# Kernel tuning notes

Hardware: AMD Instinct MI355X
Metric: run time of the kernel (lower is better)

## Reference

```python
import jax, jax.numpy as jnp
import numpy as np

D_MODEL = 512
NUM_HEADS = 8
D_K = D_MODEL // NUM_HEADS


def setup_inputs() -> dict:
    key = jax.random.key(0)
    ks = jax.random.split(key, 11)
    B, S = 2, 4096
    s = 1.0 / np.sqrt(D_MODEL)
    inp = {
        "q": jax.random.normal(ks[0], (B, S, D_MODEL), jnp.float32),
        "k": jax.random.normal(ks[1], (B, S, D_MODEL), jnp.float32),
        "v": jax.random.normal(ks[2], (B, S, D_MODEL), jnp.float32),
        "Wq": jax.random.normal(ks[3], (D_MODEL, D_MODEL), jnp.float32) * s,
        "bq": jnp.zeros((D_MODEL,), jnp.float32),
        "Wk": jax.random.normal(ks[4], (D_MODEL, D_MODEL), jnp.float32) * s,
        "bk": jnp.zeros((D_MODEL,), jnp.float32),
        "Wv": jax.random.normal(ks[5], (D_MODEL, D_MODEL), jnp.float32) * s,
        "bv": jnp.zeros((D_MODEL,), jnp.float32),
        "Wo": jax.random.normal(ks[6], (D_MODEL, D_MODEL), jnp.float32) * s,
        "bo": jnp.zeros((D_MODEL,), jnp.float32),
    }
    return inp


def reference(q, k, v, Wq, bq, Wk, bk, Wv, bv, Wo, bo):
    B, S, _ = q.shape
    # Linear projections (torch Linear: x @ W.T + b)
    def proj(x, W, b):
        y = jnp.einsum("bsd,ed->bse", x, W) + b
        return y.reshape(B, -1, NUM_HEADS, D_K).transpose(0, 2, 1, 3)  # [B,H,S,d_k]

    qh = proj(q, Wq, bq)
    kh = proj(k, Wk, bk)
    vh = proj(v, Wv, bv)

    scale = 1.0 / np.sqrt(D_K).astype(np.float32)
    scores = jnp.einsum("bhqd,bhkd->bhqk", qh, kh) * scale  # [B,H,S,S]
    attn = jax.nn.softmax(scores, axis=-1)
    ctx = jnp.einsum("bhqk,bhkd->bhqd", attn, vh)  # [B,H,S,d_k]
    ctx = ctx.transpose(0, 2, 1, 3).reshape(B, -1, D_MODEL)
    out = jnp.einsum("bsd,ed->bse", ctx, Wo) + bo
    return out
```

## Files before the change

### kernel.cpp

```cpp
#include <hip/hip_runtime.h>
#include <hip/hip_bf16.h>
#include <stdint.h>


typedef float  floatx4 __attribute__((ext_vector_type(4)));
typedef __bf16 bf16x8  __attribute__((ext_vector_type(8)));
typedef short  shortx4 __attribute__((ext_vector_type(4)));

#define MFMA16(a, b, c) __builtin_amdgcn_mfma_f32_16x16x32_bf16((a), (b), (c), 0, 0, 0)

#define QSCALE 0.1803368801111244f

__device__ __forceinline__ short f2bf(float f) {
  union { float f; uint32_t u; } a; a.f = f;
  uint32_t u = a.u;
  u += 0x7fffu + ((u >> 16) & 1u);
  return (short)(u >> 16);
}

__device__ __forceinline__ void stage16(const short* g, short* l) {
  __builtin_amdgcn_global_load_lds(
      (const __attribute__((address_space(1))) void*)g,
      (__attribute__((address_space(3))) void*)l, 16, 0, 0);
}

__global__ __launch_bounds__(256) void cvt3_kernel(const float* __restrict__ q,
                                                   const float* __restrict__ k,
                                                   const float* __restrict__ v,
                                                   short* __restrict__ out, int n4) {
  const int which = blockIdx.y;
  const float* in = which == 0 ? q : which == 1 ? k : v;
  short* o = out + (size_t)which * (size_t)n4 * 4;
  int i = blockIdx.x * 256 + threadIdx.x;
  if (i < n4) {
    float4 f = reinterpret_cast<const float4*>(in)[i];
    shortx4 s;
    s.x = f2bf(f.x); s.y = f2bf(f.y); s.z = f2bf(f.z); s.w = f2bf(f.w);
    reinterpret_cast<shortx4*>(o)[i] = s;
  }
}

__global__ __launch_bounds__(256) void cvtw_kernel(const float* __restrict__ w0,
                                                   const float* __restrict__ w1,
                                                   const float* __restrict__ w2,
                                                   const float* __restrict__ w3,
                                                   short* __restrict__ out, int n4) {
  const int which = blockIdx.y;
  const float* in = which == 0 ? w0 : which == 1 ? w1 : which == 2 ? w2 : w3;
  short* o = out + (size_t)which * (size_t)n4 * 4;
  int i = blockIdx.x * 256 + threadIdx.x;
  if (i < n4) {
    float4 f = reinterpret_cast<const float4*>(in)[i];
    shortx4 s;
    s.x = f2bf(f.x); s.y = f2bf(f.y); s.z = f2bf(f.z); s.w = f2bf(f.w);
    reinterpret_cast<shortx4*>(o)[i] = s;
  }
}

__global__ __launch_bounds__(256) void proj3_kernel(
    const short* __restrict__ xq, const short* __restrict__ xk, const short* __restrict__ xv,
    const short* __restrict__ wq, const short* __restrict__ wk, const short* __restrict__ wv,
    const float* __restrict__ bq, const float* __restrict__ bk, const float* __restrict__ bv,
    short* __restrict__ Qh, short* __restrict__ KV) {
  const int which = blockIdx.z;
  const short* A = which == 0 ? xq : which == 1 ? xk : xv;
  const short* W = which == 0 ? wq : which == 1 ? wk : wv;
  const float* bias = which == 0 ? bq : which == 1 ? bk : bv;

  __shared__ __align__(16) short sA[2][4096];
  __shared__ __align__(16) short sB[2][2048];

  const int K = 512;
  const int tid = threadIdx.x;
  const int lane = tid & 63;
  const int wave = tid >> 6;
  const int l15 = lane & 15;
  const int quad = lane >> 4;
  const int tileM = blockIdx.x * 128;
  const int tileN = blockIdx.y * 64;

  const int srow = tid >> 2;
  const int fr = (srow ^ (srow >> 2)) & 3;
  const int sq = ((tid & 3) ^ fr) * 8;
  const short* As0 = A + (size_t)(tileM + srow) * K + sq;
  const short* As1 = As0 + (size_t)64 * K;
  const short* Bs  = W + (size_t)(tileN + srow) * K + sq;
  const int ldw = wave * 512;

  const int fl = (l15 ^ (l15 >> 2)) & 3;
  const int qsw = (quad ^ fl) * 8;
  const int ra0 = (wave * 32 + l15) * 32 + qsw;
  const int ra1 = ra0 + 512;
  const int rb0 = l15 * 32 + qsw;

  floatx4 acc[2][4];
#pragma unroll
  for (int mt = 0; mt < 2; ++mt)
#pragma unroll
    for (int nt = 0; nt < 4; ++nt) acc[mt][nt] = (floatx4){0.f, 0.f, 0.f, 0.f};

  stage16(As0, &sA[0][ldw]);
  stage16(As1, &sA[0][2048 + ldw]);
  stage16(Bs,  &sB[0][ldw]);

#pragma unroll 2
  for (int t = 0; t < 16; ++t) {
    __syncthreads();
    if (t != 15) {
      const int kk = (t + 1) * 32;
      short* a_ld = &sA[(t + 1) & 1][ldw];
      stage16(As0 + kk, a_ld);
      stage16(As1 + kk, a_ld + 2048);
      stage16(Bs + kk, &sB[(t + 1) & 1][ldw]);
    }
    const short* sa = sA[t & 1];
    const short* sb = sB[t & 1];
    bf16x8 a0 = *(const bf16x8*)&sa[ra0];
    bf16x8 a1 = *(const bf16x8*)&sa[ra1];
#pragma unroll
    for (int nt = 0; nt < 4; ++nt) {
      bf16x8 wf = *(const bf16x8*)&sb[rb0 + nt * 512];
      acc[0][nt] = MFMA16(a0, wf, acc[0][nt]);
      acc[1][nt] = MFMA16(a1, wf, acc[1][nt]);
    }
  }

#pragma unroll
  for (int mt = 0; mt < 2; ++mt) {
    const int rowbase = tileM + wave * 32 + mt * 16 + quad * 4;
    const int b = rowbase >> 12, s = rowbase & 4095;
    const int g = s >> 5;
    if (which == 0) {
#pragma unroll
      for (int nt = 0; nt < 4; ++nt) {
        const int col = tileN + nt * 16 + l15;
        const int h = col >> 6, d = col & 63;
        const float bc = bias[col];
#pragma unroll
        for (int r = 0; r < 4; ++r) {
          const int row = rowbase + r;
          const int ss = row & 4095;
          Qh[(size_t)((b * 8 + h) * 4096 + ss) * 64 + d] = f2bf((acc[mt][nt][r] + bc) * QSCALE);
        }
      }
    } else if (which == 1) {
      const int key = s & 31;
      const int t = key >> 4;
      const int l15b = key & 15;
#pragma unroll
      for (int nt = 0; nt < 4; ++nt) {
        const int col = tileN + nt * 16 + l15;
        const int h = col >> 6, dd = col & 63;
        const int ks = dd >> 5, quadk = (dd >> 3) & 3, jj = dd & 7;
        const float bc = bias[col];
        const size_t base = ((size_t)(b * 8 + h) * 128 + g) * 4096 +
                            (size_t)(t * 2 + ks) * 512 + (size_t)quadk * 128 + jj;
#pragma unroll
        for (int r = 0; r < 4; ++r)
          KV[base + (size_t)(l15b + r) * 8] = f2bf(acc[mt][nt][r] + bc);
      }
    } else {
      const int p32 = s & 31;
      const int l0 = ((p32 & 15) >> 2) * 8 + (p32 >> 4) * 4;
      const int quadv = l0 >> 3, jv = l0 & 7;
#pragma unroll
      for (int nt = 0; nt < 4; ++nt) {
        const int col = tileN + nt * 16 + l15;
        const int h = col >> 6, dd = col & 63;
        const int dt = dd >> 4, l15v = dd & 15;
        const float bc = bias[col];
        shortx4 p;
        p.x = f2bf(acc[mt][nt][0] + bc);
        p.y = f2bf(acc[mt][nt][1] + bc);
        p.z = f2bf(acc[mt][nt][2] + bc);
        p.w = f2bf(acc[mt][nt][3] + bc);
        *(shortx4*)(KV + ((size_t)(b * 8 + h) * 128 + g) * 4096 + 2048 +
                    (size_t)dt * 512 + (size_t)quadv * 128 + (size_t)l15v * 8 + jv) = p;
      }
    }
  }
}

__global__ __launch_bounds__(256) void proj_o_kernel(
    const short* __restrict__ A, const short* __restrict__ W,
    const float* __restrict__ bias, float* __restrict__ out) {
  __shared__ __align__(16) short sA[2][4096];
  __shared__ __align__(16) short sB[2][2048];

  const int K = 512;
  const int tid = threadIdx.x;
  const int lane = tid & 63;
  const int wave = tid >> 6;
  const int l15 = lane & 15;
  const int quad = lane >> 4;
  const int tileM = blockIdx.x * 128;
  const int tileN = blockIdx.y * 64;

  const int srow = tid >> 2;
  const int fr = (srow ^ (srow >> 2)) & 3;
  const int sq = ((tid & 3) ^ fr) * 8;
  const short* As0 = A + (size_t)(tileM + srow) * K + sq;
  const short* As1 = As0 + (size_t)64 * K;
  const short* Bs  = W + (size_t)(tileN + srow) * K + sq;
  const int ldw = wave * 512;

  const int fl = (l15 ^ (l15 >> 2)) & 3;
  const int qsw = (quad ^ fl) * 8;
  const int ra0 = (wave * 32 + l15) * 32 + qsw;
  const int ra1 = ra0 + 512;
  const int rb0 = l15 * 32 + qsw;

  floatx4 acc[2][4];
#pragma unroll
  for (int mt = 0; mt < 2; ++mt)
#pragma unroll
    for (int nt = 0; nt < 4; ++nt) acc[mt][nt] = (floatx4){0.f, 0.f, 0.f, 0.f};

  stage16(As0, &sA[0][ldw]);
  stage16(As1, &sA[0][2048 + ldw]);
  stage16(Bs,  &sB[0][ldw]);

#pragma unroll 2
  for (int t = 0; t < 16; ++t) {
    __syncthreads();
    if (t != 15) {
      const int kk = (t + 1) * 32;
      short* a_ld = &sA[(t + 1) & 1][ldw];
      stage16(As0 + kk, a_ld);
      stage16(As1 + kk, a_ld + 2048);
      stage16(Bs + kk, &sB[(t + 1) & 1][ldw]);
    }
    const short* sa = sA[t & 1];
    const short* sb = sB[t & 1];
    bf16x8 a0 = *(const bf16x8*)&sa[ra0];
    bf16x8 a1 = *(const bf16x8*)&sa[ra1];
#pragma unroll
    for (int nt = 0; nt < 4; ++nt) {
      bf16x8 wf = *(const bf16x8*)&sb[rb0 + nt * 512];
      acc[0][nt] = MFMA16(a0, wf, acc[0][nt]);
      acc[1][nt] = MFMA16(a1, wf, acc[1][nt]);
    }
  }

#pragma unroll
  for (int mt = 0; mt < 2; ++mt) {
    const int rowbase = tileM + wave * 32 + mt * 16 + quad * 4;
#pragma unroll
    for (int nt = 0; nt < 4; ++nt) {
      const int col = tileN + nt * 16 + l15;
      const float bc = bias[col];
#pragma unroll
      for (int r = 0; r < 4; ++r) out[(size_t)(rowbase + r) * 512 + col] = acc[mt][nt][r] + bc;
    }
  }
}

__global__ __launch_bounds__(512) void flash_kernel(
    const short* __restrict__ Qh, const short* __restrict__ KV,
    short* __restrict__ ctx) {
  __shared__ __align__(16) short sKV[2][8192];
  __shared__ float comb[4][64][34];

  const int id = blockIdx.x;
  const int xcd = id & 7;
  const int j = id >> 3;
  const int bh = xcd + ((j >> 5) << 3);
  const int qtile = j & 31;

  const int tid = threadIdx.x;
  const int wave = tid >> 6;
  const int lane = tid & 63;
  const int l15 = lane & 15;
  const int quad = lane >> 4;
  const int wq = wave & 3;
  const int half = wave >> 2;
  const int qrow0 = qtile * 128 + wq * 32;

  bf16x8 qf[2][2];
#pragma unroll
  for (int nt = 0; nt < 2; ++nt) {
    const short* Qb = Qh + (size_t)(bh * 4096 + qrow0 + nt * 16 + l15) * 64 + quad * 8;
    qf[nt][0] = *(const bf16x8*)(Qb);
    qf[nt][1] = *(const bf16x8*)(Qb + 32);
  }

  bf16x8 ones;
  {
    union { short s[8]; bf16x8 v; } u;
#pragma unroll
    for (int i = 0; i < 8; ++i) u.s[i] = (short)0x3F80;
    ones = u.v;
  }

  const short* KVb = KV + (size_t)bh * (128 * 4096);
  const short* sg = KVb + wave * 512 + lane * 8;
  const int ldw = wave * 512;

  const floatx4 FZ = (floatx4){0.f, 0.f, 0.f, 0.f};
  floatx4 o[2][4];
  floatx4 lacc[2];
#pragma unroll
  for (int nt = 0; nt < 2; ++nt) {
    lacc[nt] = FZ;
#pragma unroll
    for (int dt = 0; dt < 4; ++dt) o[nt][dt] = FZ;
  }

  stage16(sg, &sKV[0][ldw]);
  stage16(sg + 4096, &sKV[0][ldw + 4096]);

#define COMPUTE(S) do {                                                         \
    bf16x8 ka[2][2], vf[4];                                                     \
    ka[0][0] = *(const bf16x8*)&(S)[av];                                        \
    ka[0][1] = *(const bf16x8*)&(S)[av + 512];                                  \
    ka[1][0] = *(const bf16x8*)&(S)[av + 1024];                                 \
    ka[1][1] = *(const bf16x8*)&(S)[av + 1536];                                 \
    vf[0] = *(const bf16x8*)&(S)[av + 2048];                                    \
    vf[1] = *(const bf16x8*)&(S)[av + 2560];                                    \
    vf[2] = *(const bf16x8*)&(S)[av + 3072];                                    \
    vf[3] = *(const bf16x8*)&(S)[av + 3584];                                    \
    floatx4 st[2][2];                                                           \
    _Pragma("unroll")                                                           \
    for (int nt = 0; nt < 2; ++nt)                                              \
      _Pragma("unroll")                                                         \
      for (int t = 0; t < 2; ++t)                                               \
        st[nt][t] = MFMA16(ka[t][1], qf[nt][1], MFMA16(ka[t][0], qf[nt][0], FZ)); \
    bf16x8 pb[2];                                                               \
    _Pragma("unroll")                                                           \
    for (int nt = 0; nt < 2; ++nt) {                                            \
      float p[8];                                                               \
      _Pragma("unroll")                                                         \
      for (int t = 0; t < 2; ++t)                                               \
        _Pragma("unroll")                                                       \
        for (int r = 0; r < 4; ++r) p[t * 4 + r] = __builtin_amdgcn_exp2f(st[nt][t][r]); \
      union { __hip_bfloat162 h2[4]; bf16x8 v8; } u;                            \
      u.h2[0] = __float22bfloat162_rn(float2{p[0], p[1]});                      \
      u.h2[1] = __float22bfloat162_rn(float2{p[2], p[3]});                      \
      u.h2[2] = __float22bfloat162_rn(float2{p[4], p[5]});                      \
      u.h2[3] = __float22bfloat162_rn(float2{p[6], p[7]});                      \
      pb[nt] = u.v8;                                                            \
    }                                                                           \
    _Pragma("unroll")                                                           \
    for (int nt = 0; nt < 2; ++nt) {                                            \
      lacc[nt] = MFMA16(ones, pb[nt], lacc[nt]);                                \
      _Pragma("unroll")                                                         \
      for (int dt = 0; dt < 4; ++dt)                                            \
        o[nt][dt] = MFMA16(vf[dt], pb[nt], o[nt][dt]);                          \
    }                                                                           \
  } while (0)

  const int av = lane * 8;

  for (int it = 0; it < 64; ++it) {
    __syncthreads();

    if (it != 63) {
      const short* gs = sg + (size_t)(2 * it + 2) * 4096;
      short* ld = &sKV[(it + 1) & 1][ldw];
      stage16(gs, ld);
      stage16(gs + 4096, ld + 4096);
    }

    const short* S = sKV[it & 1] + (half << 12);
    COMPUTE(S);
  }
#undef COMPUTE

  __syncthreads();
  if (half) {
    float* cb = comb[wq][lane];
#pragma unroll
    for (int nt = 0; nt < 2; ++nt) {
#pragma unroll
      for (int dt = 0; dt < 4; ++dt)
#pragma unroll
        for (int r = 0; r < 4; ++r) cb[nt * 16 + dt * 4 + r] = o[nt][dt][r];
      cb[32 + nt] = lacc[nt][0];
    }
  }
  __syncthreads();
  if (!half) {
    const float* cb = comb[wq][lane];
    const int b = bh >> 3, h = bh & 7;
#pragma unroll
    for (int nt = 0; nt < 2; ++nt) {
      const float inv = 1.0f / (lacc[nt][0] + cb[32 + nt]);
      const int row = qrow0 + nt * 16 + l15;
      short* cp = ctx + (size_t)(b * 4096 + row) * 512 + h * 64 + quad * 4;
#pragma unroll
      for (int dt = 0; dt < 4; ++dt) {
        union { __hip_bfloat162 h2[2]; shortx4 s4; } u;
        u.h2[0] = __float22bfloat162_rn(
            float2{(o[nt][dt][0] + cb[nt * 16 + dt * 4 + 0]) * inv,
                   (o[nt][dt][1] + cb[nt * 16 + dt * 4 + 1]) * inv});
        u.h2[1] = __float22bfloat162_rn(
            float2{(o[nt][dt][2] + cb[nt * 16 + dt * 4 + 2]) * inv,
                   (o[nt][dt][3] + cb[nt * 16 + dt * 4 + 3]) * inv});
        *(shortx4*)(cp + dt * 16) = u.s4;
      }
    }
  }
}

extern "C" void kernel_launch(void* const* d_in, const int* in_sizes, int n_in,
                              void* d_out, int out_size, void* d_ws, size_t ws_size,
                              hipStream_t stream) {
  const float* q  = (const float*)d_in[0];
  const float* k  = (const float*)d_in[1];
  const float* v  = (const float*)d_in[2];
  const float* Wq = (const float*)d_in[3];
  const float* bq = (const float*)d_in[4];
  const float* Wk = (const float*)d_in[5];
  const float* bk = (const float*)d_in[6];
  const float* Wv = (const float*)d_in[7];
  const float* bv = (const float*)d_in[8];
  const float* Wo = (const float*)d_in[9];
  const float* bo = (const float*)d_in[10];

  const int XN = 2 * 4096 * 512;
  const int WN = 512 * 512;

  short* ws  = (short*)d_ws;
  short* xqb = ws;
  short* xkb = ws + (size_t)XN;
  short* xvb = ws + (size_t)2 * XN;
  short* wqb = ws + (size_t)3 * XN;
  short* wkb = wqb + WN;
  short* wvb = wkb + WN;
  short* wob = wvb + WN;
  short* Qh  = wob + WN;
  short* KVf = Qh + (size_t)XN;
  short* ctx = xqb;

  dim3 cg(XN / 4 / 256, 3);
  cvt3_kernel<<<cg, 256, 0, stream>>>(q, k, v, xqb, XN / 4);
  dim3 wg(WN / 4 / 256, 4);
  cvtw_kernel<<<wg, 256, 0, stream>>>(Wq, Wk, Wv, Wo, wqb, WN / 4);

  dim3 pg(64, 8, 3);
  proj3_kernel<<<pg, 256, 0, stream>>>(xqb, xkb, xvb, wqb, wkb, wvb,
                                       bq, bk, bv, Qh, KVf);

  flash_kernel<<<512, 512, 0, stream>>>(Qh, KVf, ctx);

  dim3 og(64, 8);
  proj_o_kernel<<<og, 256, 0, stream>>>(ctx, wob, bo, (float*)d_out);
}
```

Before: 212.7 us.

## Merge conversion kernels, widen GEMM N tiles, split flash KV four ways

Merges the activation and weight bf16 conversion kernels into one launch. Doubles the N tile of the projection GEMMs to 128 columns, which halves the grid and reuses each A fragment across more MFMAs at the cost of more accumulator registers. Moves the flash kernel to 1024 threads with a four-way split of each KV block across wave groups, and combines the partial outputs through a tree reduction in LDS that reuses the KV buffer. This raises in-flight work per block but adds reduction syncs and register pressure under the launch_bounds(1024, 8) hint.

```diff
diff --git a/kernel.cpp b/kernel.cpp
--- a/kernel.cpp
+++ b/kernel.cpp
@@ -24,37 +24,33 @@
       (__attribute__((address_space(3))) void*)l, 16, 0, 0);
 }
 
-__global__ __launch_bounds__(256) void cvt3_kernel(const float* __restrict__ q,
-                                                   const float* __restrict__ k,
-                                                   const float* __restrict__ v,
-                                                   short* __restrict__ out, int n4) {
-  const int which = blockIdx.y;
-  const float* in = which == 0 ? q : which == 1 ? k : v;
-  short* o = out + (size_t)which * (size_t)n4 * 4;
-  int i = blockIdx.x * 256 + threadIdx.x;
-  if (i < n4) {
-    float4 f = reinterpret_cast<const float4*>(in)[i];
-    shortx4 s;
-    s.x = f2bf(f.x); s.y = f2bf(f.y); s.z = f2bf(f.z); s.w = f2bf(f.w);
-    reinterpret_cast<shortx4*>(o)[i] = s;
-  }
-}
-
-__global__ __launch_bounds__(256) void cvtw_kernel(const float* __restrict__ w0,
-                                                   const float* __restrict__ w1,
-                                                   const float* __restrict__ w2,
-                                                   const float* __restrict__ w3,
-                                                   short* __restrict__ out, int n4) {
-  const int which = blockIdx.y;
-  const float* in = which == 0 ? w0 : which == 1 ? w1 : which == 2 ? w2 : w3;
-  short* o = out + (size_t)which * (size_t)n4 * 4;
-  int i = blockIdx.x * 256 + threadIdx.x;
-  if (i < n4) {
-    float4 f = reinterpret_cast<const float4*>(in)[i];
-    shortx4 s;
-    s.x = f2bf(f.x); s.y = f2bf(f.y); s.z = f2bf(f.z); s.w = f2bf(f.w);
-    reinterpret_cast<shortx4*>(o)[i] = s;
-  }
+__global__ __launch_bounds__(256) void cvt_all_kernel(
+    const float* __restrict__ q, const float* __restrict__ k, const float* __restrict__ v,
+    const float* __restrict__ Wq, const float* __restrict__ Wk,
+    const float* __restrict__ Wv, const float* __restrict__ Wo,
+    short* __restrict__ act, short* __restrict__ wts) {
+  const int A4 = (2 * 4096 * 512) / 4;
+  const int W4 = (512 * 512) / 4;
+  const int i = blockIdx.x * 256 + threadIdx.x;
+  const float* in;
+  short* out;
+  int j;
+  if (i < 3 * A4) {
+    const int which = i >> 20;
+    j = i - which * A4;
+    in = which == 0 ? q : which == 1 ? k : v;
+    out = act + (size_t)which * (size_t)A4 * 4;
+  } else {
+    const int t = i - 3 * A4;
+    const int which = t >> 16;
+    j = t - which * W4;
+    in = which == 0 ? Wq : which == 1 ? Wk : which == 2 ? Wv : Wo;
+    out = wts + (size_t)which * (size_t)W4 * 4;
+  }
+  float4 f = reinterpret_cast<const float4*>(in)[j];
+  shortx4 s;
+  s.x = f2bf(f.x); s.y = f2bf(f.y); s.z = f2bf(f.z); s.w = f2bf(f.w);
+  reinterpret_cast<shortx4*>(out)[j] = s;
 }
 
 __global__ __launch_bounds__(256) void proj3_kernel(
@@ -68,7 +64,7 @@
   const float* bias = which == 0 ? bq : which == 1 ? bk : bv;
 
   __shared__ __align__(16) short sA[2][4096];
-  __shared__ __align__(16) short sB[2][2048];
+  __shared__ __align__(16) short sB[2][4096];
 
   const int K = 512;
   const int tid = threadIdx.x;
@@ -77,14 +73,15 @@
   const int l15 = lane & 15;
   const int quad = lane >> 4;
   const int tileM = blockIdx.x * 128;
-  const int tileN = blockIdx.y * 64;
+  const int tileN = blockIdx.y * 128;
 
   const int srow = tid >> 2;
   const int fr = (srow ^ (srow >> 2)) & 3;
   const int sq = ((tid & 3) ^ fr) * 8;
   const short* As0 = A + (size_t)(tileM + srow) * K + sq;
   const short* As1 = As0 + (size_t)64 * K;
-  const short* Bs  = W + (size_t)(tileN + srow) * K + sq;
+  const short* Bs0 = W + (size_t)(tileN + srow) * K + sq;
+  const short* Bs1 = Bs0 + (size_t)64 * K;
   const int ldw = wave * 512;
 
   const int fl = (l15 ^ (l15 >> 2)) & 3;
@@ -93,15 +90,16 @@
   const int ra1 = ra0 + 512;
   const int rb0 = l15 * 32 + qsw;
 
-  floatx4 acc[2][4];
+  floatx4 acc[2][8];
 #pragma unroll
   for (int mt = 0; mt < 2; ++mt)
 #pragma unroll
-    for (int nt = 0; nt < 4; ++nt) acc[mt][nt] = (floatx4){0.f, 0.f, 0.f, 0.f};
+    for (int nt = 0; nt < 8; ++nt) acc[mt][nt] = (floatx4){0.f, 0.f, 0.f, 0.f};
 
   stage16(As0, &sA[0][ldw]);
   stage16(As1, &sA[0][2048 + ldw]);
-  stage16(Bs,  &sB[0][ldw]);
+  stage16(Bs0, &sB[0][ldw]);
+  stage16(Bs1, &sB[0][2048 + ldw]);
 
 #pragma unroll 2
   for (int t = 0; t < 16; ++t) {
@@ -109,16 +107,18 @@
     if (t != 15) {
       const int kk = (t + 1) * 32;
       short* a_ld = &sA[(t + 1) & 1][ldw];
+      short* b_ld = &sB[(t + 1) & 1][ldw];
       stage16(As0 + kk, a_ld);
       stage16(As1 + kk, a_ld + 2048);
-      stage16(Bs + kk, &sB[(t + 1) & 1][ldw]);
+      stage16(Bs0 + kk, b_ld);
+      stage16(Bs1 + kk, b_ld + 2048);
     }
     const short* sa = sA[t & 1];
     const short* sb = sB[t & 1];
     bf16x8 a0 = *(const bf16x8*)&sa[ra0];
     bf16x8 a1 = *(const bf16x8*)&sa[ra1];
 #pragma unroll
-    for (int nt = 0; nt < 4; ++nt) {
+    for (int nt = 0; nt < 8; ++nt) {
       bf16x8 wf = *(const bf16x8*)&sb[rb0 + nt * 512];
       acc[0][nt] = MFMA16(a0, wf, acc[0][nt]);
       acc[1][nt] = MFMA16(a1, wf, acc[1][nt]);
@@ -132,7 +132,7 @@
     const int g = s >> 5;
     if (which == 0) {
 #pragma unroll
-      for (int nt = 0; nt < 4; ++nt) {
+      for (int nt = 0; nt < 8; ++nt) {
         const int col = tileN + nt * 16 + l15;
         const int h = col >> 6, d = col & 63;
         const float bc = bias[col];
@@ -145,16 +145,16 @@
       }
     } else if (which == 1) {
       const int key = s & 31;
-      const int t = key >> 4;
+      const int tt = key >> 4;
       const int l15b = key & 15;
 #pragma unroll
-      for (int nt = 0; nt < 4; ++nt) {
+      for (int nt = 0; nt < 8; ++nt) {
         const int col = tileN + nt * 16 + l15;
         const int h = col >> 6, dd = col & 63;
         const int ks = dd >> 5, quadk = (dd >> 3) & 3, jj = dd & 7;
         const float bc = bias[col];
         const size_t base = ((size_t)(b * 8 + h) * 128 + g) * 4096 +
-                            (size_t)(t * 2 + ks) * 512 + (size_t)quadk * 128 + jj;
+                            (size_t)(tt * 2 + ks) * 512 + (size_t)quadk * 128 + jj;
 #pragma unroll
         for (int r = 0; r < 4; ++r)
           KV[base + (size_t)(l15b + r) * 8] = f2bf(acc[mt][nt][r] + bc);
@@ -164,7 +164,7 @@
       const int l0 = ((p32 & 15) >> 2) * 8 + (p32 >> 4) * 4;
       const int quadv = l0 >> 3, jv = l0 & 7;
 #pragma unroll
-      for (int nt = 0; nt < 4; ++nt) {
+      for (int nt = 0; nt < 8; ++nt) {
         const int col = tileN + nt * 16 + l15;
         const int h = col >> 6, dd = col & 63;
         const int dt = dd >> 4, l15v = dd & 15;
@@ -185,7 +185,7 @@
     const short* __restrict__ A, const short* __restrict__ W,
     const float* __restrict__ bias, float* __restrict__ out) {
   __shared__ __align__(16) short sA[2][4096];
-  __shared__ __align__(16) short sB[2][2048];
+  __shared__ __align__(16) short sB[2][4096];
 
   const int K = 512;
   const int tid = threadIdx.x;
@@ -194,14 +194,15 @@
   const int l15 = lane & 15;
   const int quad = lane >> 4;
   const int tileM = blockIdx.x * 128;
-  const int tileN = blockIdx.y * 64;
+  const int tileN = blockIdx.y * 128;
 
   const int srow = tid >> 2;
   const int fr = (srow ^ (srow >> 2)) & 3;
   const int sq = ((tid & 3) ^ fr) * 8;
   const short* As0 = A + (size_t)(tileM + srow) * K + sq;
   const short* As1 = As0 + (size_t)64 * K;
-  const short* Bs  = W + (size_t)(tileN + srow) * K + sq;
+  const short* Bs0 = W + (size_t)(tileN + srow) * K + sq;
+  const short* Bs1 = Bs0 + (size_t)64 * K;
   const int ldw = wave * 512;
 
   const int fl = (l15 ^ (l15 >> 2)) & 3;
@@ -210,15 +211,16 @@
   const int ra1 = ra0 + 512;
   const int rb0 = l15 * 32 + qsw;
 
-  floatx4 acc[2][4];
+  floatx4 acc[2][8];
 #pragma unroll
   for (int mt = 0; mt < 2; ++mt)
 #pragma unroll
-    for (int nt = 0; nt < 4; ++nt) acc[mt][nt] = (floatx4){0.f, 0.f, 0.f, 0.f};
+    for (int nt = 0; nt < 8; ++nt) acc[mt][nt] = (floatx4){0.f, 0.f, 0.f, 0.f};
 
   stage16(As0, &sA[0][ldw]);
   stage16(As1, &sA[0][2048 + ldw]);
-  stage16(Bs,  &sB[0][ldw]);
+  stage16(Bs0, &sB[0][ldw]);
+  stage16(Bs1, &sB[0][2048 + ldw]);
 
 #pragma unroll 2
   for (int t = 0; t < 16; ++t) {
@@ -226,16 +228,18 @@
     if (t != 15) {
       const int kk = (t + 1) * 32;
       short* a_ld = &sA[(t + 1) & 1][ldw];
+      short* b_ld = &sB[(t + 1) & 1][ldw];
       stage16(As0 + kk, a_ld);
       stage16(As1 + kk, a_ld + 2048);
-      stage16(Bs + kk, &sB[(t + 1) & 1][ldw]);
+      stage16(Bs0 + kk, b_ld);
+      stage16(Bs1 + kk, b_ld + 2048);
     }
     const short* sa = sA[t & 1];
     const short* sb = sB[t & 1];
     bf16x8 a0 = *(const bf16x8*)&sa[ra0];
     bf16x8 a1 = *(const bf16x8*)&sa[ra1];
 #pragma unroll
-    for (int nt = 0; nt < 4; ++nt) {
+    for (int nt = 0; nt < 8; ++nt) {
       bf16x8 wf = *(const bf16x8*)&sb[rb0 + nt * 512];
       acc[0][nt] = MFMA16(a0, wf, acc[0][nt]);
       acc[1][nt] = MFMA16(a1, wf, acc[1][nt]);
@@ -246,7 +250,7 @@
   for (int mt = 0; mt < 2; ++mt) {
     const int rowbase = tileM + wave * 32 + mt * 16 + quad * 4;
 #pragma unroll
-    for (int nt = 0; nt < 4; ++nt) {
+    for (int nt = 0; nt < 8; ++nt) {
       const int col = tileN + nt * 16 + l15;
       const float bc = bias[col];
 #pragma unroll
@@ -255,11 +259,11 @@
   }
 }
 
-__global__ __launch_bounds__(512) void flash_kernel(
+__global__ __launch_bounds__(1024, 8) void flash_kernel(
     const short* __restrict__ Qh, const short* __restrict__ KV,
     short* __restrict__ ctx) {
-  __shared__ __align__(16) short sKV[2][8192];
-  __shared__ float comb[4][64][34];
+  __shared__ __align__(16) short sKV[2][16384];
+  __shared__ float comb_l[3][4][64][2];
 
   const int id = blockIdx.x;
   const int xcd = id & 7;
@@ -272,9 +276,9 @@
   const int lane = tid & 63;
   const int l15 = lane & 15;
   const int quad = lane >> 4;
-  const int wq = wave & 3;
-  const int half = wave >> 2;
-  const int qrow0 = qtile * 128 + wq * 32;
+  const int qg = wave & 3;
+  const int ks = wave >> 2;
+  const int qrow0 = qtile * 128 + qg * 32;
 
   bf16x8 qf[2][2];
 #pragma unroll
@@ -293,8 +297,8 @@
   }
 
   const short* KVb = KV + (size_t)bh * (128 * 4096);
-  const short* sg = KVb + wave * 512 + lane * 8;
-  const int ldw = wave * 512;
+  const short* sg = KVb + wave * 1024 + lane * 8;
+  const int ldw = wave * 1024;
 
   const floatx4 FZ = (floatx4){0.f, 0.f, 0.f, 0.f};
   floatx4 o[2][4];
@@ -307,7 +311,7 @@
   }
 
   stage16(sg, &sKV[0][ldw]);
-  stage16(sg + 4096, &sKV[0][ldw + 4096]);
+  stage16(sg + 512, &sKV[0][ldw + 512]);
 
 #define COMPUTE(S) do {                                                         \
     bf16x8 ka[2][2], vf[4];                                                     \
@@ -351,51 +355,85 @@
 
   const int av = lane * 8;
 
-  for (int it = 0; it < 64; ++it) {
+  for (int it = 0; it < 32; ++it) {
     __syncthreads();
 
-    if (it != 63) {
-      const short* gs = sg + (size_t)(2 * it + 2) * 4096;
+    if (it != 31) {
+      const short* gs = sg + (size_t)(it + 1) * 16384;
       short* ld = &sKV[(it + 1) & 1][ldw];
       stage16(gs, ld);
-      stage16(gs + 4096, ld + 4096);
-    }
-
-    const short* S = sKV[it & 1] + (half << 12);
+      stage16(gs + 512, ld + 512);
+    }
+
+    const short* S = &sKV[it & 1][ks << 12];
     COMPUTE(S);
   }
 #undef COMPUTE
 
   __syncthreads();
-  if (half) {
-    float* cb = comb[wq][lane];
+  float* cb = (float*)sKV;
+  const int slot = (qg * 64 + lane) * 32;
+  const int rot = lane & 7;
+
+  if (ks == 1 || ks == 3) {
+    float* dst = cb + (ks == 3 ? 8192 : 0) + slot;
+#pragma unroll
+    for (int nt = 0; nt < 2; ++nt)
+#pragma unroll
+      for (int dt = 0; dt < 4; ++dt) {
+        const int c = nt * 4 + dt;
+        *(floatx4*)(dst + ((c ^ rot) & 7) * 4) = o[nt][dt];
+      }
+  }
+  if (ks) {
+    comb_l[ks - 1][qg][lane][0] = lacc[0][0];
+    comb_l[ks - 1][qg][lane][1] = lacc[1][0];
+  }
+  __syncthreads();
+  if (ks == 0 || ks == 2) {
+    const float* src = cb + (ks == 2 ? 8192 : 0) + slot;
+#pragma unroll
+    for (int nt = 0; nt < 2; ++nt)
+#pragma unroll
+      for (int dt = 0; dt < 4; ++dt) {
+        const int c = nt * 4 + dt;
+        o[nt][dt] += *(const floatx4*)(src + ((c ^ rot) & 7) * 4);
+      }
+  }
+  __syncthreads();
+  if (ks == 2) {
+    float* dst = cb + slot;
+#pragma unroll
+    for (int nt = 0; nt < 2; ++nt)
+#pragma unroll
+      for (int dt = 0; dt < 4; ++dt) {
+        const int c = nt * 4 + dt;
+        *(floatx4*)(dst + ((c ^ rot) & 7) * 4) = o[nt][dt];
+      }
+  }
+  __syncthreads();
+  if (ks == 0) {
+    const float* src = cb + slot;
+#pragma unroll
+    for (int nt = 0; nt < 2; ++nt)
+#pragma unroll
+      for (int dt = 0; dt < 4; ++dt) {
+        const int c = nt * 4 + dt;
+        o[nt][dt] += *(const floatx4*)(src + ((c ^ rot) & 7) * 4);
+      }
+    const int b = bh >> 3, h = bh & 7;
 #pragma unroll
     for (int nt = 0; nt < 2; ++nt) {
-#pragma unroll
-      for (int dt = 0; dt < 4; ++dt)
-#pragma unroll
-        for (int r = 0; r < 4; ++r) cb[nt * 16 + dt * 4 + r] = o[nt][dt][r];
-      cb[32 + nt] = lacc[nt][0];
-    }
-  }
-  __syncthreads();
-  if (!half) {
-    const float* cb = comb[wq][lane];
-    const int b = bh >> 3, h = bh & 7;
-#pragma unroll
-    for (int nt = 0; nt < 2; ++nt) {
-      const float inv = 1.0f / (lacc[nt][0] + cb[32 + nt]);
+      const float lt = lacc[nt][0] + comb_l[0][qg][lane][nt] +
+                       comb_l[1][qg][lane][nt] + comb_l[2][qg][lane][nt];
+      const float inv = 1.0f / lt;
       const int row = qrow0 + nt * 16 + l15;
       short* cp = ctx + (size_t)(b * 4096 + row) * 512 + h * 64 + quad * 4;
 #pragma unroll
       for (int dt = 0; dt < 4; ++dt) {
         union { __hip_bfloat162 h2[2]; shortx4 s4; } u;
-        u.h2[0] = __float22bfloat162_rn(
-            float2{(o[nt][dt][0] + cb[nt * 16 + dt * 4 + 0]) * inv,
-                   (o[nt][dt][1] + cb[nt * 16 + dt * 4 + 1]) * inv});
-        u.h2[1] = __float22bfloat162_rn(
-            float2{(o[nt][dt][2] + cb[nt * 16 + dt * 4 + 2]) * inv,
-                   (o[nt][dt][3] + cb[nt * 16 + dt * 4 + 3]) * inv});
+        u.h2[0] = __float22bfloat162_rn(float2{o[nt][dt][0] * inv, o[nt][dt][1] * inv});
+        u.h2[1] = __float22bfloat162_rn(float2{o[nt][dt][2] * inv, o[nt][dt][3] * inv});
         *(shortx4*)(cp + dt * 16) = u.s4;
       }
     }
@@ -432,17 +470,16 @@
   short* KVf = Qh + (size_t)XN;
   short* ctx = xqb;
 
-  dim3 cg(XN / 4 / 256, 3);
-  cvt3_kernel<<<cg, 256, 0, stream>>>(q, k, v, xqb, XN / 4);
-  dim3 wg(WN / 4 / 256, 4);
-  cvtw_kernel<<<wg, 256, 0, stream>>>(Wq, Wk, Wv, Wo, wqb, WN / 4);
-
-  dim3 pg(64, 8, 3);
+  const int A4 = XN / 4, W4 = WN / 4;
+  cvt_all_kernel<<<(3 * A4 + 4 * W4) / 256, 256, 0, stream>>>(
+      q, k, v, Wq, Wk, Wv, Wo, xqb, wqb);
+
+  dim3 pg(64, 4, 3);
   proj3_kernel<<<pg, 256, 0, stream>>>(xqb, xkb, xvb, wqb, wkb, wvb,
                                        bq, bk, bv, Qh, KVf);
 
-  flash_kernel<<<512, 512, 0, stream>>>(Qh, KVf, ctx);
-
-  dim3 og(64, 8);
+  flash_kernel<<<512, 1024, 0, stream>>>(Qh, KVf, ctx);
+
+  dim3 og(64, 4);
   proj_o_kernel<<<og, 256, 0, stream>>>(ctx, wob, bo, (float*)d_out);
 }
```

Measured after the change: 644.0 us. +202.7%, slower.
